# Kernel optimization log

Measured on AMD Instinct MI355X. Metric: run time of the kernel, lower is better.

The kernel has to match this reference:

```python
import jax, jax.numpy as jnp
import numpy as np

DIM = 1024
H = 16
HD = DIM // H  # 64
EPS = 1e-5


def setup_inputs() -> dict:
    key = jax.random.key(0)
    ks = jax.random.split(key, 10)
    B, S = 2, 2048
    lim_h = 1.0 / np.sqrt(HD)
    lim_d = 1.0 / np.sqrt(DIM)
    u = lambda k, shape, lim: jax.random.uniform(k, shape, jnp.float32, -lim, lim)
    return {
        "q": jax.random.normal(ks[0], (B, S, DIM), jnp.float32),
        "k": jax.random.normal(ks[1], (B, S, DIM), jnp.float32),
        "v": jax.random.normal(ks[2], (B, S, DIM), jnp.float32),
        "wq1": u(ks[3], (H, HD, HD), lim_h),
        "wk1": u(ks[4], (H, HD, HD), lim_h),
        "wq2": u(ks[5], (H, HD, HD), lim_h),
        "wk2": u(ks[6], (H, HD, HD), lim_h),
        "wv": u(ks[7], (H, HD, HD), lim_h),
        "wo": u(ks[8], (DIM, DIM), lim_d),
        "gain": jnp.float32(0.3),
    }


def reference(q, k, v, wq1, wk1, wq2, wk2, wv, wo, gain):
    B, S, D = q.shape
    h, hd = wq1.shape[0], wq1.shape[1]
    scale = jnp.sqrt(jnp.asarray(hd, jnp.float32))
    # split heads: [B,S,H,hd]
    qh = q.reshape(B, S, h, hd)
    kh = k.reshape(B, S, h, hd)
    vh = v.reshape(B, S, h, hd)
    # per-head linear y = x @ W^T (torch Linear convention)
    q1 = jnp.einsum('bshd,hed->bshe', qh, wq1)
    k1 = jnp.einsum('bshd,hed->bshe', kh, wk1)
    q2 = jnp.einsum('bshd,hed->bshe', qh, wq2)
    k2 = jnp.einsum('bshd,hed->bshe', kh, wk2)
    vp = jnp.einsum('bshd,hed->bshe', vh, wv)
    # dual attention scores [B,H,S,S]
    s1 = jnp.einsum('bshe,bthe->bhst', q1, k1) / scale
    s2 = jnp.einsum('bshe,bthe->bhst', q2, k2) / scale
    attn = jax.nn.softmax(s1, axis=-1) - gain * jax.nn.softmax(s2, axis=-1)
    o = jnp.einsum('bhst,bthe->bshe', attn, vp)  # [B,S,H,hd]
    # group_norm(x, num_groups=S) on [B,S,hd]: per-(b,s) normalize over hd, no affine
    mean = jnp.mean(o, axis=-1, keepdims=True)
    var = jnp.mean(jnp.square(o - mean), axis=-1, keepdims=True)
    o = (o - mean) / jnp.sqrt(var + EPS)
    out = o.reshape(B, S, D) @ wo.T
    return out
```

## Files before the change

### kernel.cpp

```cpp
#include <hip/hip_runtime.h>
#include <hip/hip_bf16.h>
#include <cstdint>

#define B_ 2
#define S_ 2048
#define D_ 1024
#define H_ 16

typedef __bf16 bf16;
typedef _Float16 f16;
typedef bf16 bf16x8 __attribute__((ext_vector_type(8)));
typedef f16 f16x8 __attribute__((ext_vector_type(8)));
typedef f16 f16x4 __attribute__((ext_vector_type(4)));
typedef float floatx4 __attribute__((ext_vector_type(4)));
typedef uint32_t u32x4 __attribute__((ext_vector_type(4)));
typedef uint32_t u32x2 __attribute__((ext_vector_type(2)));

__device__ __forceinline__ floatx4 mfma_bf(bf16x8 a, bf16x8 b, floatx4 c) {
    return __builtin_amdgcn_mfma_f32_16x16x32_bf16(a, b, c, 0, 0, 0);
}
__device__ __forceinline__ floatx4 mfma_h(f16x8 a, f16x8 b, floatx4 c) {
    return __builtin_amdgcn_mfma_f32_16x16x32_f16(a, b, c, 0, 0, 0);
}

__device__ __forceinline__ uint32_t pkz(float a, float b) {
    return __builtin_bit_cast(uint32_t, __builtin_amdgcn_cvt_pkrtz(a, b));
}

__device__ __forceinline__ void lds_barrier() {
    asm volatile("s_waitcnt lgkmcnt(0)" ::: "memory");
    __builtin_amdgcn_s_barrier();
}

__device__ __forceinline__ bool detect_f32(const void* gainp) {
    float g = *(const float*)gainp;
    return fabsf(g - 0.3f) < 1e-2f;
}
__device__ __forceinline__ float ldf(const void* base, size_t i, bool f32m) {
    return f32m ? ((const float*)base)[i] : (float)((const bf16*)base)[i];
}
struct f8 { floatx4 a, b; };
__device__ __forceinline__ f8 ld8f(const void* base, size_t i, bool f32m) {
    f8 r;
    if (f32m) {
        const floatx4* p = (const floatx4*)((const float*)base + i);
        r.a = p[0]; r.b = p[1];
    } else {
        bf16x8 v = *(const bf16x8*)((const bf16*)base + i);
        r.a = (floatx4){(float)v[0], (float)v[1], (float)v[2], (float)v[3]};
        r.b = (floatx4){(float)v[4], (float)v[5], (float)v[6], (float)v[7]};
    }
    return r;
}
__device__ __forceinline__ f16x8 cvt8h(const f8& x) {
    u32x4 t;
    t[0] = pkz(x.a[0], x.a[1]); t[1] = pkz(x.a[2], x.a[3]);
    t[2] = pkz(x.b[0], x.b[1]); t[3] = pkz(x.b[2], x.b[3]);
    return __builtin_bit_cast(f16x8, t);
}
__device__ __forceinline__ void ld_raw(const void* base, size_t i, bool f32m,
                                       u32x4& c0, u32x4& c1) {
    if (f32m) {
        const u32x4* p = (const u32x4*)((const float*)base + i);
        c0 = p[0]; c1 = p[1];
    } else {
        c0 = *(const u32x4*)((const bf16*)base + i);
    }
}
__device__ __forceinline__ f16x8 raw_to_h(u32x4 c0, u32x4 c1, bool f32m) {
    u32x4 t;
    if (f32m) {
        floatx4 a = __builtin_bit_cast(floatx4, c0);
        floatx4 b = __builtin_bit_cast(floatx4, c1);
        t[0] = pkz(a[0], a[1]); t[1] = pkz(a[2], a[3]);
        t[2] = pkz(b[0], b[1]); t[3] = pkz(b[2], b[3]);
    } else {
        bf16x8 v = __builtin_bit_cast(bf16x8, c0);
        t[0] = pkz((float)v[0], (float)v[1]);
        t[1] = pkz((float)v[2], (float)v[3]);
        t[2] = pkz((float)v[4], (float)v[5]);
        t[3] = pkz((float)v[6], (float)v[7]);
    }
    return __builtin_bit_cast(f16x8, t);
}
__device__ __forceinline__ void split8(const f8& x, bf16x8& h, bf16x8& l) {
    #pragma unroll
    for (int j = 0; j < 4; ++j) {
        float v = x.a[j]; bf16 hh = (bf16)v; h[j] = hh; l[j] = (bf16)(v - (float)hh);
        float u = x.b[j]; bf16 gg = (bf16)u; h[4 + j] = gg; l[4 + j] = (bf16)(u - (float)gg);
    }
}
__device__ __forceinline__ floatx4 mfma3(bf16x8 ah, bf16x8 al, bf16x8 bh, bf16x8 bl,
                                         floatx4 c) {
    c = mfma_bf(ah, bh, c);
    c = mfma_bf(al, bh, c);
    c = mfma_bf(ah, bl, c);
    return c;
}

__global__ __launch_bounds__(256) void combine_kernel(
    const void* __restrict__ wq1, const void* __restrict__ wk1,
    const void* __restrict__ wq2, const void* __restrict__ wk2,
    const void* __restrict__ gainp, float* __restrict__ M1t, float* __restrict__ M2t)
{
    const bool f32m = detect_f32(gainp);
    const int p = blockIdx.x & 1, dq = blockIdx.x >> 1, h = blockIdx.y;
    const int tid = threadIdx.x;
    __shared__ float wa[4096], wb16[1024];
    const void* wqp = p ? wq2 : wq1;
    const void* wkp = p ? wk2 : wk1;
    float* Mt = p ? M2t : M1t;
    for (int i = tid; i < 4096; i += 256)
        wa[i] = ldf(wqp, (size_t)h * 4096 + i, f32m);
    for (int i = tid; i < 1024; i += 256) {
        int e = i >> 4, dd = i & 15;
        wb16[i] = ldf(wkp, (size_t)h * 4096 + e * 64 + dq * 16 + dd, f32m);
    }
    __syncthreads();
    for (int r = 0; r < 4; ++r) {
        int idx = r * 256 + tid;
        int dl = idx >> 6, f = idx & 63;
        float acc = 0.f;
        #pragma unroll 8
        for (int e = 0; e < 64; ++e)
            acc += wa[e * 64 + f] * wb16[e * 16 + dl];
        Mt[(size_t)h * 4096 + (dq * 16 + dl) * 64 + f] = acc * 0.125f;
    }
}

__global__ __launch_bounds__(256) void attn_kernel(
    const void* __restrict__ qin, const void* __restrict__ kin,
    const void* __restrict__ vin, const void* __restrict__ wv,
    const float* __restrict__ M1t, const float* __restrict__ M2t,
    const void* __restrict__ gainp, f16* __restrict__ on)
{
    const bool f32m = detect_f32(gainp);
    const float gain = f32m ? *(const float*)gainp : (float)(*(const bf16*)gainp);
    const int s0 = blockIdx.x * 64;
    const int h = blockIdx.y, b = blockIdx.z;
    const int tid = threadIdx.x;
    const int w = tid >> 6, lane = tid & 63;
    const int l15 = lane & 15, quad = lane >> 4;

    __shared__ __align__(16) f16 smem[4 * 64 * 72];
    f16 (*ktile)[72]  = (f16(*)[72])smem;
    f16 (*vtile)[72]  = (f16(*)[72])(smem + 4608);
    f16 (*ptile1)[72] = (f16(*)[72])(smem + 9216);
    f16 (*ptile2)[72] = (f16(*)[72])(smem + 13824);

    {
        size_t qr = (size_t)(b * S_ + s0 + w * 16 + l15) * D_ + h * 64;
        f8 x0 = ld8f(qin, qr + quad * 8, f32m);
        f8 x1 = ld8f(qin, qr + 32 + quad * 8, f32m);
        bf16x8 aq0h, aq0l, aq1h, aq1l;
        split8(x0, aq0h, aq0l);
        split8(x1, aq1h, aq1l);
        #pragma unroll
        for (int p = 0; p < 2; ++p) {
            const float* Mt = p ? M2t : M1t;
            f16 (*qt)[72] = p ? vtile : ktile;
            #pragma unroll
            for (int nt = 0; nt < 4; ++nt) {
                size_t mr = (size_t)h * 4096 + (size_t)(nt * 16 + l15) * 64;
                f8 m0 = ld8f(Mt, mr + quad * 8, true);
                f8 m1 = ld8f(Mt, mr + 32 + quad * 8, true);
                bf16x8 b0h, b0l, b1h, b1l;
                split8(m0, b0h, b0l);
                split8(m1, b1h, b1l);
                floatx4 acc = {0.f, 0.f, 0.f, 0.f};
                acc = mfma3(aq0h, aq0l, b0h, b0l, acc);
                acc = mfma3(aq1h, aq1l, b1h, b1l, acc);
                #pragma unroll
                for (int r = 0; r < 4; ++r)
                    qt[w * 16 + quad * 4 + r][nt * 16 + l15] = (f16)acc[r];
            }
        }
    }
    f16x8 q1a = *(const f16x8*)&ktile[w * 16 + l15][quad * 8];
    f16x8 q1b = *(const f16x8*)&ktile[w * 16 + l15][quad * 8 + 32];
    f16x8 q2a = *(const f16x8*)&vtile[w * 16 + l15][quad * 8];
    f16x8 q2b = *(const f16x8*)&vtile[w * 16 + l15][quad * 8 + 32];

    floatx4 o1[4], o2[4];
    float l1s = 0.f, l2s = 0.f;
    #pragma unroll
    for (int i = 0; i < 4; ++i) {
        o1[i] = (floatx4){0.f, 0.f, 0.f, 0.f};
        o2[i] = (floatx4){0.f, 0.f, 0.f, 0.f};
    }

    const size_t inbase = (size_t)b * S_ * D_ + h * 64;
    const int row0 = (tid) >> 3,       ch0 = (tid) & 7;
    const int row1 = (256 + tid) >> 3, ch1 = (256 + tid) & 7;

    u32x4 kr0a, kr0b, kr1a, kr1b, vr0a, vr0b, vr1a, vr1b;
    {
        size_t g0 = inbase + (size_t)row0 * D_ + ch0 * 8;
        size_t g1 = inbase + (size_t)row1 * D_ + ch1 * 8;
        ld_raw(kin, g0, f32m, kr0a, kr0b);
        ld_raw(vin, g0, f32m, vr0a, vr0b);
        ld_raw(kin, g1, f32m, kr1a, kr1b);
        ld_raw(vin, g1, f32m, vr1a, vr1b);
    }

    for (int kt = 0; kt < S_ / 64; ++kt) {
        lds_barrier();
        {
            *(f16x8*)&ktile[row0][ch0 * 8] = raw_to_h(kr0a, kr0b, f32m);
            f16x8 vh0 = raw_to_h(vr0a, vr0b, f32m);
            int tc0 = (row0 + 8 * ch0) & 63;
            #pragma unroll
            for (int j = 0; j < 8; ++j) vtile[ch0 * 8 + j][tc0] = vh0[j];
            *(f16x8*)&ktile[row1][ch1 * 8] = raw_to_h(kr1a, kr1b, f32m);
            f16x8 vh1 = raw_to_h(vr1a, vr1b, f32m);
            int tc1 = (row1 + 8 * ch1) & 63;
            #pragma unroll
            for (int j = 0; j < 8; ++j) vtile[ch1 * 8 + j][tc1] = vh1[j];
        }
        if (kt + 1 < S_ / 64) {
            const int t0n = (kt + 1) * 64;
            size_t g0 = inbase + (size_t)(t0n + row0) * D_ + ch0 * 8;
            size_t g1 = inbase + (size_t)(t0n + row1) * D_ + ch1 * 8;
            ld_raw(kin, g0, f32m, kr0a, kr0b);
            ld_raw(vin, g0, f32m, vr0a, vr0b);
            ld_raw(kin, g1, f32m, kr1a, kr1b);
            ld_raw(vin, g1, f32m, vr1a, vr1b);
        }
        lds_barrier();

        floatx4 s1t[4], s2t[4];
        #pragma unroll
        for (int jt = 0; jt < 4; ++jt) {
            f16x8 b0 = *(const f16x8*)&ktile[jt * 16 + l15][quad * 8];
            f16x8 b1 = *(const f16x8*)&ktile[jt * 16 + l15][quad * 8 + 32];
            floatx4 a = {0.f, 0.f, 0.f, 0.f};
            a = mfma_h(b0, q1a, a);
            a = mfma_h(b1, q1b, a);
            s1t[jt] = a;
            floatx4 c = {0.f, 0.f, 0.f, 0.f};
            c = mfma_h(b0, q2a, c);
            c = mfma_h(b1, q2b, c);
            s2t[jt] = c;
        }

        f16x8 bv0[4], bv1[4];
        #pragma unroll
        for (int et = 0; et < 4; ++et) {
            int e = et * 16 + l15;
            int g0 = ((quad + (e >> 3)) & 7) * 8;
            int g1 = ((quad + 4 + (e >> 3)) & 7) * 8;
            bv0[et] = *(const f16x8*)&vtile[e][g0];
            bv1[et] = *(const f16x8*)&vtile[e][g1];
        }

        #pragma unroll
        for (int jt = 0; jt < 4; ++jt) {
            float p0 = __expf(fminf(s1t[jt][0], 30.f));
            float p1 = __expf(fminf(s1t[jt][1], 30.f));
            float p2 = __expf(fminf(s1t[jt][2], 30.f));
            float p3 = __expf(fminf(s1t[jt][3], 30.f));
            l1s += (p0 + p1) + (p2 + p3);
            u32x2 pw; pw[0] = pkz(p0, p1); pw[1] = pkz(p2, p3);
            *(u32x2*)&ptile1[w * 16 + l15][jt * 16 + quad * 4] = pw;
        }
        f16x8 p1a = *(const f16x8*)&ptile1[w * 16 + l15][quad * 8];
        f16x8 p1b = *(const f16x8*)&ptile1[w * 16 + l15][quad * 8 + 32];
        #pragma unroll
        for (int jt = 0; jt < 4; ++jt) {
            float p0 = __expf(fminf(s2t[jt][0], 30.f));
            float p1 = __expf(fminf(s2t[jt][1], 30.f));
            float p2 = __expf(fminf(s2t[jt][2], 30.f));
            float p3 = __expf(fminf(s2t[jt][3], 30.f));
            l2s += (p0 + p1) + (p2 + p3);
            u32x2 pw; pw[0] = pkz(p0, p1); pw[1] = pkz(p2, p3);
            *(u32x2*)&ptile2[w * 16 + l15][jt * 16 + quad * 4] = pw;
        }
        #pragma unroll
        for (int et = 0; et < 4; ++et) {
            o1[et] = mfma_h(bv0[et], p1a, o1[et]);
            o1[et] = mfma_h(bv1[et], p1b, o1[et]);
        }
        f16x8 p2a = *(const f16x8*)&ptile2[w * 16 + l15][quad * 8];
        f16x8 p2b = *(const f16x8*)&ptile2[w * 16 + l15][quad * 8 + 32];
        #pragma unroll
        for (int et = 0; et < 4; ++et) {
            o2[et] = mfma_h(bv0[et], p2a, o2[et]);
            o2[et] = mfma_h(bv1[et], p2b, o2[et]);
        }
    }

    l1s += __shfl_xor(l1s, 16);
    l1s += __shfl_xor(l1s, 32);
    l2s += __shfl_xor(l2s, 16);
    l2s += __shfl_xor(l2s, 32);
    float n1 = 1.0f / l1s;
    float n2 = gain / l2s;

    #pragma unroll
    for (int et = 0; et < 4; ++et) {
        float v0 = o1[et][0] * n1 - o2[et][0] * n2;
        float v1 = o1[et][1] * n1 - o2[et][1] * n2;
        float v2 = o1[et][2] * n1 - o2[et][2] * n2;
        float v3 = o1[et][3] * n1 - o2[et][3] * n2;
        u32x2 pw; pw[0] = pkz(v0, v1); pw[1] = pkz(v2, v3);
        *(u32x2*)&ptile1[w * 16 + l15][et * 16 + quad * 4] = pw;
    }
    f16x8 aoa = *(const f16x8*)&ptile1[w * 16 + l15][quad * 8];
    f16x8 aob = *(const f16x8*)&ptile1[w * 16 + l15][quad * 8 + 32];

    floatx4 of[4];
    #pragma unroll
    for (int nt = 0; nt < 4; ++nt) {
        size_t wr = (size_t)h * 4096 + (size_t)(nt * 16 + l15) * 64;
        f16x8 b0 = cvt8h(ld8f(wv, wr + quad * 8, f32m));
        f16x8 b1 = cvt8h(ld8f(wv, wr + 32 + quad * 8, f32m));
        floatx4 acc = {0.f, 0.f, 0.f, 0.f};
        acc = mfma_h(aoa, b0, acc);
        acc = mfma_h(aob, b1, acc);
        of[nt] = acc;
    }

    #pragma unroll
    for (int r = 0; r < 4; ++r) {
        float sm = 0.f, sq = 0.f;
        #pragma unroll
        for (int nt = 0; nt < 4; ++nt) { sm += of[nt][r]; sq += of[nt][r] * of[nt][r]; }
        #pragma unroll
        for (int m = 1; m < 16; m <<= 1) {
            sm += __shfl_xor(sm, m, 16);
            sq += __shfl_xor(sq, m, 16);
        }
        float mean = sm * (1.0f / 64.0f);
        float var = sq * (1.0f / 64.0f) - mean * mean;
        float rstd = rsqrtf(fmaxf(var, 0.f) + 1e-5f);
        int srow = s0 + w * 16 + quad * 4 + r;
        size_t base = (size_t)(b * S_ + srow) * D_ + h * 64;
        #pragma unroll
        for (int nt = 0; nt < 4; ++nt)
            on[base + nt * 16 + l15] = (f16)((of[nt][r] - mean) * rstd);
    }
}

__global__ __launch_bounds__(512) void ogemm_kernel(
    const f16* __restrict__ x, const void* __restrict__ wo,
    const void* __restrict__ gainp, void* __restrict__ outp)
{
    const bool f32m = detect_f32(gainp);
    const int m0 = blockIdx.x * 128;
    const int n0 = blockIdx.y * 128;
    const int tid = threadIdx.x;
    const int w = tid >> 6, lane = tid & 63;
    const int l15 = lane & 15, quad = lane >> 4;
    const int wm = w >> 2, wn = w & 3;

    __shared__ __align__(16) f16 xh[128][72], wh[128][72];

    floatx4 acc[4][2];
    #pragma unroll
    for (int mt = 0; mt < 4; ++mt)
        #pragma unroll
        for (int nt = 0; nt < 2; ++nt) acc[mt][nt] = (floatx4){0.f, 0.f, 0.f, 0.f};

    const int r0 = tid >> 3, ch = tid & 7;

    u32x4 xr0, xr1, wr0a, wr0b, wr1a, wr1b;
    {
        xr0 = *(const u32x4*)&x[(size_t)(m0 + r0) * 1024 + ch * 8];
        xr1 = *(const u32x4*)&x[(size_t)(m0 + r0 + 64) * 1024 + ch * 8];
        ld_raw(wo, (size_t)(n0 + r0) * 1024 + ch * 8, f32m, wr0a, wr0b);
        ld_raw(wo, (size_t)(n0 + r0 + 64) * 1024 + ch * 8, f32m, wr1a, wr1b);
    }

    for (int kc = 0; kc < 16; ++kc) {
        lds_barrier();
        *(f16x8*)&xh[r0][ch * 8]      = __builtin_bit_cast(f16x8, xr0);
        *(f16x8*)&xh[r0 + 64][ch * 8] = __builtin_bit_cast(f16x8, xr1);
        *(f16x8*)&wh[r0][ch * 8]      = raw_to_h(wr0a, wr0b, f32m);
        *(f16x8*)&wh[r0 + 64][ch * 8] = raw_to_h(wr1a, wr1b, f32m);
        if (kc + 1 < 16) {
            const int k1 = (kc + 1) * 64;
            xr0 = *(const u32x4*)&x[(size_t)(m0 + r0) * 1024 + k1 + ch * 8];
            xr1 = *(const u32x4*)&x[(size_t)(m0 + r0 + 64) * 1024 + k1 + ch * 8];
            ld_raw(wo, (size_t)(n0 + r0) * 1024 + k1 + ch * 8, f32m, wr0a, wr0b);
            ld_raw(wo, (size_t)(n0 + r0 + 64) * 1024 + k1 + ch * 8, f32m, wr1a, wr1b);
        }
        lds_barrier();

        f16x8 a0[4], a1[4];
        #pragma unroll
        for (int mt = 0; mt < 4; ++mt) {
            a0[mt] = *(const f16x8*)&xh[wm * 64 + mt * 16 + l15][quad * 8];
            a1[mt] = *(const f16x8*)&xh[wm * 64 + mt * 16 + l15][quad * 8 + 32];
        }
        f16x8 b0[2], b1[2];
        #pragma unroll
        for (int nt = 0; nt < 2; ++nt) {
            b0[nt] = *(const f16x8*)&wh[wn * 32 + nt * 16 + l15][quad * 8];
            b1[nt] = *(const f16x8*)&wh[wn * 32 + nt * 16 + l15][quad * 8 + 32];
        }
        #pragma unroll
        for (int mt = 0; mt < 4; ++mt)
            #pragma unroll
            for (int nt = 0; nt < 2; ++nt) {
                acc[mt][nt] = mfma_h(a0[mt], b0[nt], acc[mt][nt]);
                acc[mt][nt] = mfma_h(a1[mt], b1[nt], acc[mt][nt]);
            }
    }
    #pragma unroll
    for (int mt = 0; mt < 4; ++mt)
        #pragma unroll
        for (int nt = 0; nt < 2; ++nt)
            #pragma unroll
            for (int r = 0; r < 4; ++r) {
                size_t idx = (size_t)(m0 + wm * 64 + mt * 16 + quad * 4 + r) * 1024
                           + n0 + wn * 32 + nt * 16 + l15;
                if (f32m) ((float*)outp)[idx] = acc[mt][nt][r];
                else      ((bf16*)outp)[idx] = (bf16)acc[mt][nt][r];
            }
}

extern "C" void kernel_launch(void* const* d_in, const int* in_sizes, int n_in,
                              void* d_out, int out_size, void* d_ws, size_t ws_size,
                              hipStream_t stream)
{
    const void* q    = d_in[0];
    const void* k    = d_in[1];
    const void* v    = d_in[2];
    const void* wq1  = d_in[3];
    const void* wk1  = d_in[4];
    const void* wq2  = d_in[5];
    const void* wk2  = d_in[6];
    const void* wv   = d_in[7];
    const void* wo   = d_in[8];
    const void* gain = d_in[9];

    float* M1t = (float*)d_ws;
    float* M2t = M1t + (size_t)H_ * 4096;
    f16*   on  = (f16*)(M2t + (size_t)H_ * 4096);

    combine_kernel<<<dim3(8, H_), dim3(256), 0, stream>>>(
        wq1, wk1, wq2, wk2, gain, M1t, M2t);
    attn_kernel<<<dim3(S_ / 64, H_, B_), dim3(256), 0, stream>>>(
        q, k, v, wv, M1t, M2t, gain, on);
    ogemm_kernel<<<dim3(32, 8), dim3(512), 0, stream>>>(on, wo, gain, d_out);
}
```

Baseline: 271.2 us.

## Double-buffer LDS tiles in attention and output GEMM kernels, one barrier per tile

Both the attention kernel and the output-projection GEMM now use ping-pong shared-memory buffers. The next tile is staged into the alternate buffer while the current one is computed, which cuts the barriers per tile from two to one. The attention kernel also merges its two probability tiles into one, reordering the first P·V MFMA before the second exp pass. LDS use rises (attention 46KB, GEMM 72KB), which may lower occupancy, and reusing the single P tile depends on each wave touching only its own rows.

After: 259.4 us. -4.4%, faster.

```diff
diff --git a/kernel.cpp b/kernel.cpp
--- a/kernel.cpp
+++ b/kernel.cpp
@@ -142,11 +142,12 @@
     const int w = tid >> 6, lane = tid & 63;
     const int l15 = lane & 15, quad = lane >> 4;
 
-    __shared__ __align__(16) f16 smem[4 * 64 * 72];
-    f16 (*ktile)[72]  = (f16(*)[72])smem;
-    f16 (*vtile)[72]  = (f16(*)[72])(smem + 4608);
-    f16 (*ptile1)[72] = (f16(*)[72])(smem + 9216);
-    f16 (*ptile2)[72] = (f16(*)[72])(smem + 13824);
+    __shared__ __align__(16) f16 smem[5 * 64 * 72];
+    f16 (*kA)[72] = (f16(*)[72])smem;
+    f16 (*kB)[72] = (f16(*)[72])(smem + 4608);
+    f16 (*vA)[72] = (f16(*)[72])(smem + 9216);
+    f16 (*vB)[72] = (f16(*)[72])(smem + 13824);
+    f16 (*pt)[72] = (f16(*)[72])(smem + 18432);
 
     {
         size_t qr = (size_t)(b * S_ + s0 + w * 16 + l15) * D_ + h * 64;
@@ -158,7 +159,7 @@
         #pragma unroll
         for (int p = 0; p < 2; ++p) {
             const float* Mt = p ? M2t : M1t;
-            f16 (*qt)[72] = p ? vtile : ktile;
+            f16 (*qt)[72] = p ? vA : kA;
             #pragma unroll
             for (int nt = 0; nt < 4; ++nt) {
                 size_t mr = (size_t)h * 4096 + (size_t)(nt * 16 + l15) * 64;
@@ -176,10 +177,10 @@
             }
         }
     }
-    f16x8 q1a = *(const f16x8*)&ktile[w * 16 + l15][quad * 8];
-    f16x8 q1b = *(const f16x8*)&ktile[w * 16 + l15][quad * 8 + 32];
-    f16x8 q2a = *(const f16x8*)&vtile[w * 16 + l15][quad * 8];
-    f16x8 q2b = *(const f16x8*)&vtile[w * 16 + l15][quad * 8 + 32];
+    f16x8 q1a = *(const f16x8*)&kA[w * 16 + l15][quad * 8];
+    f16x8 q1b = *(const f16x8*)&kA[w * 16 + l15][quad * 8 + 32];
+    f16x8 q2a = *(const f16x8*)&vA[w * 16 + l15][quad * 8];
+    f16x8 q2b = *(const f16x8*)&vA[w * 16 + l15][quad * 8 + 32];
 
     floatx4 o1[4], o2[4];
     float l1s = 0.f, l2s = 0.f;
@@ -192,47 +193,35 @@
     const size_t inbase = (size_t)b * S_ * D_ + h * 64;
     const int row0 = (tid) >> 3,       ch0 = (tid) & 7;
     const int row1 = (256 + tid) >> 3, ch1 = (256 + tid) & 7;
+    const int tc0 = (row0 + 8 * ch0) & 63;
+    const int tc1 = (row1 + 8 * ch1) & 63;
 
     u32x4 kr0a, kr0b, kr1a, kr1b, vr0a, vr0b, vr1a, vr1b;
-    {
-        size_t g0 = inbase + (size_t)row0 * D_ + ch0 * 8;
-        size_t g1 = inbase + (size_t)row1 * D_ + ch1 * 8;
+
+    auto LDKV = [&](int t0n) {
+        size_t g0 = inbase + (size_t)(t0n + row0) * D_ + ch0 * 8;
+        size_t g1 = inbase + (size_t)(t0n + row1) * D_ + ch1 * 8;
         ld_raw(kin, g0, f32m, kr0a, kr0b);
         ld_raw(vin, g0, f32m, vr0a, vr0b);
         ld_raw(kin, g1, f32m, kr1a, kr1b);
         ld_raw(vin, g1, f32m, vr1a, vr1b);
-    }
-
-    for (int kt = 0; kt < S_ / 64; ++kt) {
-        lds_barrier();
-        {
-            *(f16x8*)&ktile[row0][ch0 * 8] = raw_to_h(kr0a, kr0b, f32m);
-            f16x8 vh0 = raw_to_h(vr0a, vr0b, f32m);
-            int tc0 = (row0 + 8 * ch0) & 63;
-            #pragma unroll
-            for (int j = 0; j < 8; ++j) vtile[ch0 * 8 + j][tc0] = vh0[j];
-            *(f16x8*)&ktile[row1][ch1 * 8] = raw_to_h(kr1a, kr1b, f32m);
-            f16x8 vh1 = raw_to_h(vr1a, vr1b, f32m);
-            int tc1 = (row1 + 8 * ch1) & 63;
-            #pragma unroll
-            for (int j = 0; j < 8; ++j) vtile[ch1 * 8 + j][tc1] = vh1[j];
-        }
-        if (kt + 1 < S_ / 64) {
-            const int t0n = (kt + 1) * 64;
-            size_t g0 = inbase + (size_t)(t0n + row0) * D_ + ch0 * 8;
-            size_t g1 = inbase + (size_t)(t0n + row1) * D_ + ch1 * 8;
-            ld_raw(kin, g0, f32m, kr0a, kr0b);
-            ld_raw(vin, g0, f32m, vr0a, vr0b);
-            ld_raw(kin, g1, f32m, kr1a, kr1b);
-            ld_raw(vin, g1, f32m, vr1a, vr1b);
-        }
-        lds_barrier();
-
+    };
+    auto STAGE = [&](f16 (*kt_)[72], f16 (*vt_)[72]) {
+        *(f16x8*)&kt_[row0][ch0 * 8] = raw_to_h(kr0a, kr0b, f32m);
+        f16x8 vh0 = raw_to_h(vr0a, vr0b, f32m);
+        #pragma unroll
+        for (int j = 0; j < 8; ++j) vt_[ch0 * 8 + j][tc0] = vh0[j];
+        *(f16x8*)&kt_[row1][ch1 * 8] = raw_to_h(kr1a, kr1b, f32m);
+        f16x8 vh1 = raw_to_h(vr1a, vr1b, f32m);
+        #pragma unroll
+        for (int j = 0; j < 8; ++j) vt_[ch1 * 8 + j][tc1] = vh1[j];
+    };
+    auto COMPUTE = [&](f16 (*kt_)[72], f16 (*vt_)[72]) {
         floatx4 s1t[4], s2t[4];
         #pragma unroll
         for (int jt = 0; jt < 4; ++jt) {
-            f16x8 b0 = *(const f16x8*)&ktile[jt * 16 + l15][quad * 8];
-            f16x8 b1 = *(const f16x8*)&ktile[jt * 16 + l15][quad * 8 + 32];
+            f16x8 b0 = *(const f16x8*)&kt_[jt * 16 + l15][quad * 8];
+            f16x8 b1 = *(const f16x8*)&kt_[jt * 16 + l15][quad * 8 + 32];
             floatx4 a = {0.f, 0.f, 0.f, 0.f};
             a = mfma_h(b0, q1a, a);
             a = mfma_h(b1, q1b, a);
@@ -242,17 +231,15 @@
             c = mfma_h(b1, q2b, c);
             s2t[jt] = c;
         }
-
         f16x8 bv0[4], bv1[4];
         #pragma unroll
         for (int et = 0; et < 4; ++et) {
             int e = et * 16 + l15;
             int g0 = ((quad + (e >> 3)) & 7) * 8;
             int g1 = ((quad + 4 + (e >> 3)) & 7) * 8;
-            bv0[et] = *(const f16x8*)&vtile[e][g0];
-            bv1[et] = *(const f16x8*)&vtile[e][g1];
-        }
-
+            bv0[et] = *(const f16x8*)&vt_[e][g0];
+            bv1[et] = *(const f16x8*)&vt_[e][g1];
+        }
         #pragma unroll
         for (int jt = 0; jt < 4; ++jt) {
             float p0 = __expf(fminf(s1t[jt][0], 30.f));
@@ -261,10 +248,15 @@
             float p3 = __expf(fminf(s1t[jt][3], 30.f));
             l1s += (p0 + p1) + (p2 + p3);
             u32x2 pw; pw[0] = pkz(p0, p1); pw[1] = pkz(p2, p3);
-            *(u32x2*)&ptile1[w * 16 + l15][jt * 16 + quad * 4] = pw;
-        }
-        f16x8 p1a = *(const f16x8*)&ptile1[w * 16 + l15][quad * 8];
-        f16x8 p1b = *(const f16x8*)&ptile1[w * 16 + l15][quad * 8 + 32];
+            *(u32x2*)&pt[w * 16 + l15][jt * 16 + quad * 4] = pw;
+        }
+        f16x8 p1a = *(const f16x8*)&pt[w * 16 + l15][quad * 8];
+        f16x8 p1b = *(const f16x8*)&pt[w * 16 + l15][quad * 8 + 32];
+        #pragma unroll
+        for (int et = 0; et < 4; ++et) {
+            o1[et] = mfma_h(bv0[et], p1a, o1[et]);
+            o1[et] = mfma_h(bv1[et], p1b, o1[et]);
+        }
         #pragma unroll
         for (int jt = 0; jt < 4; ++jt) {
             float p0 = __expf(fminf(s2t[jt][0], 30.f));
@@ -273,20 +265,34 @@
             float p3 = __expf(fminf(s2t[jt][3], 30.f));
             l2s += (p0 + p1) + (p2 + p3);
             u32x2 pw; pw[0] = pkz(p0, p1); pw[1] = pkz(p2, p3);
-            *(u32x2*)&ptile2[w * 16 + l15][jt * 16 + quad * 4] = pw;
-        }
-        #pragma unroll
-        for (int et = 0; et < 4; ++et) {
-            o1[et] = mfma_h(bv0[et], p1a, o1[et]);
-            o1[et] = mfma_h(bv1[et], p1b, o1[et]);
-        }
-        f16x8 p2a = *(const f16x8*)&ptile2[w * 16 + l15][quad * 8];
-        f16x8 p2b = *(const f16x8*)&ptile2[w * 16 + l15][quad * 8 + 32];
+            *(u32x2*)&pt[w * 16 + l15][jt * 16 + quad * 4] = pw;
+        }
+        f16x8 p2a = *(const f16x8*)&pt[w * 16 + l15][quad * 8];
+        f16x8 p2b = *(const f16x8*)&pt[w * 16 + l15][quad * 8 + 32];
         #pragma unroll
         for (int et = 0; et < 4; ++et) {
             o2[et] = mfma_h(bv0[et], p2a, o2[et]);
             o2[et] = mfma_h(bv1[et], p2b, o2[et]);
         }
+    };
+
+    LDKV(0);
+    lds_barrier();
+    STAGE(kA, vA);
+    LDKV(64);
+    lds_barrier();
+
+    for (int kt = 0; kt < S_ / 64; kt += 2) {
+        STAGE(kB, vB);
+        if (kt + 2 < S_ / 64) LDKV((kt + 2) * 64);
+        COMPUTE(kA, vA);
+        lds_barrier();
+        if (kt + 2 < S_ / 64) {
+            STAGE(kA, vA);
+            if (kt + 3 < S_ / 64) LDKV((kt + 3) * 64);
+        }
+        COMPUTE(kB, vB);
+        lds_barrier();
     }
 
     l1s += __shfl_xor(l1s, 16);
@@ -303,10 +309,10 @@
         float v2 = o1[et][2] * n1 - o2[et][2] * n2;
         float v3 = o1[et][3] * n1 - o2[et][3] * n2;
         u32x2 pw; pw[0] = pkz(v0, v1); pw[1] = pkz(v2, v3);
-        *(u32x2*)&ptile1[w * 16 + l15][et * 16 + quad * 4] = pw;
-    }
-    f16x8 aoa = *(const f16x8*)&ptile1[w * 16 + l15][quad * 8];
-    f16x8 aob = *(const f16x8*)&ptile1[w * 16 + l15][quad * 8 + 32];
+        *(u32x2*)&pt[w * 16 + l15][et * 16 + quad * 4] = pw;
+    }
+    f16x8 aoa = *(const f16x8*)&pt[w * 16 + l15][quad * 8];
+    f16x8 aob = *(const f16x8*)&pt[w * 16 + l15][quad * 8 + 32];
 
     floatx4 of[4];
     #pragma unroll
@@ -353,7 +359,8 @@
     const int l15 = lane & 15, quad = lane >> 4;
     const int wm = w >> 2, wn = w & 3;
 
-    __shared__ __align__(16) f16 xh[128][72], wh[128][72];
+    __shared__ __align__(16) f16 xhA[128][72], whA[128][72];
+    __shared__ __align__(16) f16 xhB[128][72], whB[128][72];
 
     floatx4 acc[4][2];
     #pragma unroll
@@ -364,28 +371,20 @@
     const int r0 = tid >> 3, ch = tid & 7;
 
     u32x4 xr0, xr1, wr0a, wr0b, wr1a, wr1b;
-    {
-        xr0 = *(const u32x4*)&x[(size_t)(m0 + r0) * 1024 + ch * 8];
-        xr1 = *(const u32x4*)&x[(size_t)(m0 + r0 + 64) * 1024 + ch * 8];
-        ld_raw(wo, (size_t)(n0 + r0) * 1024 + ch * 8, f32m, wr0a, wr0b);
-        ld_raw(wo, (size_t)(n0 + r0 + 64) * 1024 + ch * 8, f32m, wr1a, wr1b);
-    }
-
-    for (int kc = 0; kc < 16; ++kc) {
-        lds_barrier();
+    auto LD = [&](int kc) {
+        const int k1 = kc * 64;
+        xr0 = *(const u32x4*)&x[(size_t)(m0 + r0) * 1024 + k1 + ch * 8];
+        xr1 = *(const u32x4*)&x[(size_t)(m0 + r0 + 64) * 1024 + k1 + ch * 8];
+        ld_raw(wo, (size_t)(n0 + r0) * 1024 + k1 + ch * 8, f32m, wr0a, wr0b);
+        ld_raw(wo, (size_t)(n0 + r0 + 64) * 1024 + k1 + ch * 8, f32m, wr1a, wr1b);
+    };
+    auto STAGE = [&](f16 (*xh)[72], f16 (*wh)[72]) {
         *(f16x8*)&xh[r0][ch * 8]      = __builtin_bit_cast(f16x8, xr0);
         *(f16x8*)&xh[r0 + 64][ch * 8] = __builtin_bit_cast(f16x8, xr1);
         *(f16x8*)&wh[r0][ch * 8]      = raw_to_h(wr0a, wr0b, f32m);
         *(f16x8*)&wh[r0 + 64][ch * 8] = raw_to_h(wr1a, wr1b, f32m);
-        if (kc + 1 < 16) {
-            const int k1 = (kc + 1) * 64;
-            xr0 = *(const u32x4*)&x[(size_t)(m0 + r0) * 1024 + k1 + ch * 8];
-            xr1 = *(const u32x4*)&x[(size_t)(m0 + r0 + 64) * 1024 + k1 + ch * 8];
-            ld_raw(wo, (size_t)(n0 + r0) * 1024 + k1 + ch * 8, f32m, wr0a, wr0b);
-            ld_raw(wo, (size_t)(n0 + r0 + 64) * 1024 + k1 + ch * 8, f32m, wr1a, wr1b);
-        }
-        lds_barrier();
-
+    };
+    auto COMPUTE = [&](f16 (*xh)[72], f16 (*wh)[72]) {
         f16x8 a0[4], a1[4];
         #pragma unroll
         for (int mt = 0; mt < 4; ++mt) {
@@ -405,6 +404,23 @@
                 acc[mt][nt] = mfma_h(a0[mt], b0[nt], acc[mt][nt]);
                 acc[mt][nt] = mfma_h(a1[mt], b1[nt], acc[mt][nt]);
             }
+    };
+
+    LD(0);
+    STAGE(xhA, whA);
+    LD(1);
+    lds_barrier();
+    for (int kc = 0; kc < 16; kc += 2) {
+        STAGE(xhB, whB);
+        if (kc + 2 < 16) LD(kc + 2);
+        COMPUTE(xhA, whA);
+        lds_barrier();
+        if (kc + 2 < 16) {
+            STAGE(xhA, whA);
+            if (kc + 3 < 16) LD(kc + 3);
+        }
+        COMPUTE(xhB, whB);
+        lds_barrier();
     }
     #pragma unroll
     for (int mt = 0; mt < 4; ++mt)
```
